# Kernel tuning notes

Measured on AMD Instinct MI355X. Metric: run time of the kernel, lower is better.

The kernel has to match this reference:

```python
import jax, jax.numpy as jnp
import numpy as np

B, S, D = 2, 2048, 1024
H = 16
HD = D // H  # 64
EPS = 1e-6
ROPE_BASE = 10000.0


def _rms_norm(x, w, eps=EPS):
    # torch nn.RMSNorm over last dim
    var = jnp.mean(jnp.square(x), axis=-1, keepdims=True)
    return x * jax.lax.rsqrt(var + eps) * w


def _rope_tables(seq_len, head_dim, base=ROPE_BASE):
    inv_freq = 1.0 / (base ** (jnp.arange(0, head_dim, 2, dtype=jnp.float32) / head_dim))
    t = jnp.arange(seq_len, dtype=jnp.float32)
    freqs = t[:, None] * inv_freq[None, :]            # [S, HD/2]
    emb = jnp.concatenate([freqs, freqs], axis=-1)    # [S, HD]
    return jnp.cos(emb), jnp.sin(emb)


def _rotate_half(x):
    x1, x2 = jnp.split(x, 2, axis=-1)
    return jnp.concatenate([-x2, x1], axis=-1)


def _apply_rope(x, cos, sin):
    # x: [B, H, S, HD]; cos/sin: [S, HD]
    return x * cos[None, None] + _rotate_half(x) * sin[None, None]


def setup_inputs() -> dict:
    key = jax.random.key(0)
    ks = jax.random.split(key, 8)
    scale = 1.0 / np.sqrt(D)
    return {
        "x": jax.random.normal(ks[0], (B, S, D), dtype=jnp.float32),
        "wq": jax.random.normal(ks[1], (D, D), dtype=jnp.float32) * scale,
        "wk": jax.random.normal(ks[2], (D, D), dtype=jnp.float32) * scale,
        "wv": jax.random.normal(ks[3], (D, D), dtype=jnp.float32) * scale,
        "wo": jax.random.normal(ks[4], (D, D), dtype=jnp.float32) * scale,
        "q_norm_w": jnp.ones((HD,), dtype=jnp.float32),
        "k_norm_w": jnp.ones((HD,), dtype=jnp.float32),
        "sink_logit": jnp.zeros((H,), dtype=jnp.float32),
    }


def reference(x, wq, wk, wv, wo, q_norm_w, k_norm_w, sink_logit):
    b, s, _ = x.shape
    # QKV projections (nn.Linear, no bias): y = x @ W^T
    q = jnp.einsum("bsd,od->bso", x, wq).reshape(b, s, H, HD)
    k = jnp.einsum("bsd,od->bso", x, wk).reshape(b, s, H, HD)
    v = jnp.einsum("bsd,od->bso", x, wv).reshape(b, s, H, HD)
    # QK RMSNorm (per head_dim)
    q = _rms_norm(q, q_norm_w)
    k = _rms_norm(k, k_norm_w)
    # [B, H, S, HD]
    q = q.transpose(0, 2, 1, 3)
    k = k.transpose(0, 2, 1, 3)
    v = v.transpose(0, 2, 1, 3)
    # full-head RoPE
    cos, sin = _rope_tables(s, HD)
    q = _apply_rope(q, cos, sin)
    k = _apply_rope(k, cos, sin)
    # manual attention with causal mask and sink softmax
    scale = HD ** -0.5
    scores = jnp.einsum("bhqd,bhkd->bhqk", q, k) * scale  # [B,H,S,S]
    causal = jnp.tril(jnp.ones((s, s), dtype=bool))
    scores = jnp.where(causal[None, None], scores, -jnp.inf)
    # sink-augmented softmax in fp32: append per-head sink logit, softmax, drop sink column
    sink = jnp.broadcast_to(sink_logit.astype(jnp.float32)[None, :, None, None], (b, H, s, 1))
    aug = jnp.concatenate([scores.astype(jnp.float32), sink], axis=-1)
    weights = jax.nn.softmax(aug, axis=-1)[..., :s].astype(scores.dtype)
    out = jnp.einsum("bhqk,bhkd->bhqd", weights, v)
    out = out.transpose(0, 2, 1, 3).reshape(b, s, D)
    return jnp.einsum("bsd,od->bso", out, wo)
```

## Files before the change

### kernel.cpp

```cpp
#include <hip/hip_runtime.h>

#define Bb 2
#define Ss 2048
#define Dd 1024
#define Hh 16
#define HDd 64
#define BS (Bb * Ss)

typedef __attribute__((ext_vector_type(8))) __bf16 bf16x8;
typedef __attribute__((ext_vector_type(8))) unsigned short u16x8;
typedef __attribute__((ext_vector_type(4))) float f32x4;

__device__ __forceinline__ unsigned short f2bf(float f) {
  union { float f; unsigned u; } v; v.f = f;
  unsigned r = v.u + 0x7fffu + ((v.u >> 16) & 1u);
  return (unsigned short)(r >> 16);
}
__device__ __forceinline__ unsigned short f2bf_fast(float f) {
  union { float f; unsigned u; } v; v.f = f;
  return (unsigned short)((v.u + 0x8000u) >> 16);
}

__device__ __forceinline__ void gl_lds16(const void* g, void* l) {
  __builtin_amdgcn_global_load_lds(
      (const __attribute__((address_space(1))) void*)g,
      (__attribute__((address_space(3))) void*)l, 16, 0, 0);
}

__global__ __launch_bounds__(256) void cast_all(
    const float4* __restrict__ x, const float4* __restrict__ wq,
    const float4* __restrict__ wk, const float4* __restrict__ wv,
    const float4* __restrict__ wo, ushort4* __restrict__ xb,
    ushort4* __restrict__ wqkvb, ushort4* __restrict__ wob,
    float* __restrict__ ct, float* __restrict__ st) {
  int i = blockIdx.x * 256 + threadIdx.x;
  const int NX4 = BS * Dd / 4;
  const int NW4 = Dd * Dd / 4;
  const float4* src;
  ushort4* dst;
  int idx;
  if (i < NX4) { src = x; dst = xb; idx = i; }
  else if ((i -= NX4) < NW4) { src = wq; dst = wqkvb; idx = i; }
  else if ((i -= NW4) < NW4) { src = wk; dst = wqkvb + NW4; idx = i; }
  else if ((i -= NW4) < NW4) { src = wv; dst = wqkvb + 2 * NW4; idx = i; }
  else if ((i -= NW4) < NW4) { src = wo; dst = wob; idx = i; }
  else if ((i -= NW4) < Ss * 32) {
    int s = i >> 5, jj = i & 31;
    float freq = __powf(10000.0f, -(float)jj * (1.0f / 32.0f));
    float cs, sn;
    sincosf((float)s * freq, &sn, &cs);
    ct[i] = cs; st[i] = sn;
    return;
  } else return;
  float4 v = src[idx];
  ushort4 o;
  o.x = f2bf(v.x); o.y = f2bf(v.y); o.z = f2bf(v.z); o.w = f2bf(v.w);
  dst[idx] = o;
}

__global__ __launch_bounds__(256, 3) void gemm_qkv(
    const unsigned short* __restrict__ A, const unsigned short* __restrict__ Bw,
    const float* __restrict__ qw, const float* __restrict__ kw,
    const float* __restrict__ ct, const float* __restrict__ st,
    unsigned short* __restrict__ Qb, unsigned short* __restrict__ Kb,
    unsigned short* __restrict__ Vt) {
  __shared__ __align__(16) unsigned short As[128 * 32];
  __shared__ __align__(16) unsigned short Bs[128 * 32];
  const int K = Dd, tid = threadIdx.x;
  const int lane = tid & 63;
  const int quad = lane >> 4;
  const int l16 = lane & 15;
  const int wave = tid >> 6;
  const int wm = (wave >> 1) * 64;
  const int wn = (wave & 1) * 64;
  const int tile_m = blockIdx.y * 128;
  const int tile_n = blockIdx.x * 128;

  const int off0 = tid * 16;
  const int off1 = 4096 + tid * 16;
  const int r0 = tid >> 2, r1 = r0 + 64;
  const int sch = (((tid & 3) ^ ((tid >> 3) & 3)) << 3);
  const int xg = ((quad ^ ((l16 >> 1) & 3)) << 3);

  const unsigned short* Ag0 = A + (size_t)(tile_m + r0) * K + sch;
  const unsigned short* Ag1 = A + (size_t)(tile_m + r1) * K + sch;
  const unsigned short* Bg0 = Bw + (size_t)(tile_n + r0) * K + sch;
  const unsigned short* Bg1 = Bw + (size_t)(tile_n + r1) * K + sch;

  f32x4 zero = {0.f, 0.f, 0.f, 0.f};
  f32x4 acc[4][4];
#pragma unroll
  for (int mi = 0; mi < 4; ++mi)
#pragma unroll
    for (int ni = 0; ni < 4; ++ni) acc[mi][ni] = zero;

  for (int k0 = 0; k0 < K; k0 += 32) {
    gl_lds16(Ag0 + k0, (char*)As + off0);
    gl_lds16(Ag1 + k0, (char*)As + off1);
    gl_lds16(Bg0 + k0, (char*)Bs + off0);
    gl_lds16(Bg1 + k0, (char*)Bs + off1);
    __syncthreads();
    bf16x8 af[4], bfv[4];
#pragma unroll
    for (int mi = 0; mi < 4; ++mi)
      af[mi] = *(const bf16x8*)&As[(wm + mi * 16 + l16) * 32 + xg];
#pragma unroll
    for (int ni = 0; ni < 4; ++ni)
      bfv[ni] = *(const bf16x8*)&Bs[(wn + ni * 16 + l16) * 32 + xg];
#pragma unroll
    for (int mi = 0; mi < 4; ++mi)
#pragma unroll
      for (int ni = 0; ni < 4; ++ni)
        acc[mi][ni] = __builtin_amdgcn_mfma_f32_16x16x32_bf16(
            af[mi], bfv[ni], acc[mi][ni], 0, 0, 0);
    __syncthreads();
  }

  const int type = blockIdx.x >> 3;
  const int h = (((blockIdx.x & 7) << 7) + wn) >> 6;
  const int bb = tile_m >> 11;
  const size_t bh = (size_t)bb * Hh + h;

  if (type == 2) {
#pragma unroll
    for (int mi = 0; mi < 4; ++mi) {
      int s0 = (tile_m + wm + mi * 16 + quad * 4) & (Ss - 1);
#pragma unroll
      for (int ni = 0; ni < 4; ++ni) {
        int d = ni * 16 + l16;
        ushort4 pv;
        pv.x = f2bf(acc[mi][ni][0]);
        pv.y = f2bf(acc[mi][ni][1]);
        pv.z = f2bf(acc[mi][ni][2]);
        pv.w = f2bf(acc[mi][ni][3]);
        *(ushort4*)&Vt[(bh * HDd + d) * Ss + s0] = pv;
      }
    }
  } else {
    const float* wnp = type ? kw : qw;
    unsigned short* Ob = type ? Kb : Qb;
    const float fscale = type ? 1.0f : 0.125f * 1.44269504f;
    float w0[4];
#pragma unroll
    for (int ni = 0; ni < 4; ++ni) w0[ni] = wnp[ni * 16 + l16];
#pragma unroll
    for (int mi = 0; mi < 4; ++mi) {
#pragma unroll
      for (int r = 0; r < 4; ++r) {
        int s = (tile_m + wm + mi * 16 + quad * 4 + r) & (Ss - 1);
        float ss2 = 0.f;
#pragma unroll
        for (int ni = 0; ni < 4; ++ni) ss2 += acc[mi][ni][r] * acc[mi][ni][r];
        ss2 += __shfl_xor(ss2, 1, 64);
        ss2 += __shfl_xor(ss2, 2, 64);
        ss2 += __shfl_xor(ss2, 4, 64);
        ss2 += __shfl_xor(ss2, 8, 64);
        float rr = rsqrtf(ss2 * (1.0f / 64.0f) + 1e-6f) * fscale;
        float c0 = ct[s * 32 + l16], c1 = ct[s * 32 + 16 + l16];
        float sn0 = st[s * 32 + l16], sn1 = st[s * 32 + 16 + l16];
#pragma unroll
        for (int ni = 0; ni < 4; ++ni) {
          float vn = acc[mi][ni][r] * rr * w0[ni];
          float vp = acc[mi][ni ^ 2][r] * rr * w0[ni ^ 2];
          float cs_ = (ni & 1) ? c1 : c0;
          float sn_ = (ni & 1) ? sn1 : sn0;
          float sg = (ni < 2) ? -1.0f : 1.0f;
          Ob[(bh * Ss + s) * HDd + ni * 16 + l16] = f2bf(vn * cs_ + sg * vp * sn_);
        }
      }
    }
  }
}

__global__ __launch_bounds__(256) void gemm_bt2(
    const unsigned short* __restrict__ A, const unsigned short* __restrict__ Bw,
    float* __restrict__ C, int M, int N, int K) {
  __shared__ __align__(16) unsigned short As[128 * 32];
  __shared__ __align__(16) unsigned short Bs[64 * 32];
  const int tid = threadIdx.x;
  const int lane = tid & 63;
  const int quad = lane >> 4;
  const int l16 = lane & 15;
  const int wave = tid >> 6;
  const int wm = (wave >> 1) * 64;
  const int wn = (wave & 1) * 32;
  const int tile_m = blockIdx.y * 128;
  const int tile_n = blockIdx.x * 64;

  const int off0 = tid * 16;
  const int off1 = 4096 + tid * 16;
  const int r0 = tid >> 2, r1 = r0 + 64;
  const int sch = (((tid & 3) ^ ((tid >> 3) & 3)) << 3);
  const int xg = ((quad ^ ((l16 >> 1) & 3)) << 3);

  const unsigned short* Ag0 = A + (size_t)(tile_m + r0) * K + sch;
  const unsigned short* Ag1 = A + (size_t)(tile_m + r1) * K + sch;
  const unsigned short* Bg0 = Bw + (size_t)(tile_n + r0) * K + sch;

  f32x4 zero = {0.f, 0.f, 0.f, 0.f};
  f32x4 acc[4][2];
#pragma unroll
  for (int mi = 0; mi < 4; ++mi)
#pragma unroll
    for (int ni = 0; ni < 2; ++ni) acc[mi][ni] = zero;

  for (int k0 = 0; k0 < K; k0 += 32) {
    gl_lds16(Ag0 + k0, (char*)As + off0);
    gl_lds16(Ag1 + k0, (char*)As + off1);
    gl_lds16(Bg0 + k0, (char*)Bs + off0);
    __syncthreads();
    bf16x8 af[4], bfv[2];
#pragma unroll
    for (int mi = 0; mi < 4; ++mi)
      af[mi] = *(const bf16x8*)&As[(wm + mi * 16 + l16) * 32 + xg];
#pragma unroll
    for (int ni = 0; ni < 2; ++ni)
      bfv[ni] = *(const bf16x8*)&Bs[(wn + ni * 16 + l16) * 32 + xg];
#pragma unroll
    for (int mi = 0; mi < 4; ++mi)
#pragma unroll
      for (int ni = 0; ni < 2; ++ni)
        acc[mi][ni] = __builtin_amdgcn_mfma_f32_16x16x32_bf16(
            af[mi], bfv[ni], acc[mi][ni], 0, 0, 0);
    __syncthreads();
  }

#pragma unroll
  for (int mi = 0; mi < 4; ++mi) {
#pragma unroll
    for (int ni = 0; ni < 2; ++ni) {
      int col = tile_n + wn + ni * 16 + l16;
#pragma unroll
      for (int r = 0; r < 4; ++r) {
        int row = tile_m + wm + mi * 16 + quad * 4 + r;
        C[(size_t)row * N + col] = acc[mi][ni][r];
      }
    }
  }
}

__global__ __launch_bounds__(256, 2) void flash(
    const unsigned short* __restrict__ Qb, const unsigned short* __restrict__ Kb,
    const unsigned short* __restrict__ Vt, const float* __restrict__ sink,
    unsigned short* __restrict__ Ob) {
  __shared__ __align__(16) unsigned short Ks[2][64 * 64];
  __shared__ __align__(16) unsigned short Vs[2][64 * 64];
  __shared__ __align__(16) unsigned short Ps[2][4][16 * 64];

  int tid = threadIdx.x, lane = tid & 63, wave = tid >> 6;
  int quad = lane >> 4, l16 = lane & 15;

  int lid = blockIdx.x;
  int h = (lid & 7) + 8 * ((lid >> 3) & 1);
  int t = (lid >> 4) & 15;
  int b = lid >> 8;
  const int qta = t, qtb = 31 - t;

  const unsigned short* Qg = Qb + ((size_t)(b * Hh + h) * Ss) * HDd;
  const unsigned short* Kg = Kb + ((size_t)(b * Hh + h) * Ss) * HDd;
  const unsigned short* Vg = Vt + ((size_t)(b * Hh + h) * HDd) * Ss;

  int off0 = tid * 16, off1 = 4096 + tid * 16;
  int sr0 = tid >> 3, sr1 = sr0 + 32;
  int sch = ((tid & 7) ^ (sr0 & 7)) * 8;
  int x0 = ((quad ^ (l16 & 7)) * 8);
  int x1 = x0 ^ 32;

  int myqa = qta * 64 + wave * 16 + l16;
  int myqb = qtb * 64 + wave * 16 + l16;

  float sk = sink[h];
  f32x4 zero = {0.f, 0.f, 0.f, 0.f};

  bf16x8 ones;
  {
    u16x8 tt;
#pragma unroll
    for (int i = 0; i < 8; ++i) tt[i] = 0x3F80;
    ones = *(bf16x8*)&tt;
  }

  const unsigned short* Qra = Qg + (size_t)myqa * HDd;
  const unsigned short* Qrb = Qg + (size_t)myqb * HDd;
  bf16x8 aq0a = *(const bf16x8*)(Qra + quad * 8);
  bf16x8 aq1a = *(const bf16x8*)(Qra + 32 + quad * 8);
  bf16x8 aq0b = *(const bf16x8*)(Qrb + quad * 8);
  bf16x8 aq1b = *(const bf16x8*)(Qrb + 32 + quad * 8);

  gl_lds16(Kg + (size_t)sr0 * 64 + sch, (char*)Ks[0] + off0);
  gl_lds16(Kg + (size_t)sr1 * 64 + sch, (char*)Ks[0] + off1);
  gl_lds16(Vg + (size_t)sr0 * Ss + sch, (char*)Vs[0] + off0);
  gl_lds16(Vg + (size_t)sr1 * Ss + sch, (char*)Vs[0] + off1);

  f32x4 Oacca[4], Oaccb[4], lacca = zero, laccb = zero;
#pragma unroll
  for (int ni = 0; ni < 4; ++ni) { Oacca[ni] = zero; Oaccb[ni] = zero; }

  __syncthreads();
  gl_lds16(Kg + (size_t)(64 + sr0) * 64 + sch, (char*)Ks[1] + off0);
  gl_lds16(Kg + (size_t)(64 + sr1) * 64 + sch, (char*)Ks[1] + off1);

  f32x4 sca[4], scb[4];
#pragma unroll
  for (int ni = 0; ni < 4; ++ni) {
    bf16x8 bk0 = *(const bf16x8*)&Ks[0][(ni * 16 + l16) * 64 + x0];
    bf16x8 bk1 = *(const bf16x8*)&Ks[0][(ni * 16 + l16) * 64 + x1];
    scb[ni] = __builtin_amdgcn_mfma_f32_16x16x32_bf16(bk0, aq0b, zero, 0, 0, 0);
    scb[ni] = __builtin_amdgcn_mfma_f32_16x16x32_bf16(bk1, aq1b, scb[ni], 0, 0, 0);
    sca[ni] = __builtin_amdgcn_mfma_f32_16x16x32_bf16(bk0, aq0a, zero, 0, 0, 0);
    sca[ni] = __builtin_amdgcn_mfma_f32_16x16x32_bf16(bk1, aq1a, sca[ni], 0, 0, 0);
  }
  if (qta == 0) {
#pragma unroll
    for (int ni = 0; ni < 4; ++ni)
#pragma unroll
      for (int r = 0; r < 4; ++r)
        if (ni * 16 + quad * 4 + r > myqa) sca[ni][r] = -1.0e38f;
  }

  char* Pwa = (char*)Ps[0][wave];
  char* Pwb = (char*)Ps[1][wave];
  const int prow = l16 * 128;
  const int psw = l16 & 7;

  for (int kt = 0; kt <= qtb; ++kt) {
    bool last = (kt == qtb);
    bool acta = (kt <= qta);
    __syncthreads();
    if (kt + 2 <= qtb) {
      gl_lds16(Kg + (size_t)((kt + 2) * 64 + sr0) * 64 + sch, (char*)Ks[kt & 1] + off0);
      gl_lds16(Kg + (size_t)((kt + 2) * 64 + sr1) * 64 + sch, (char*)Ks[kt & 1] + off1);
    }
    if (kt + 1 <= qtb) {
      gl_lds16(Vg + (size_t)sr0 * Ss + (kt + 1) * 64 + sch, (char*)Vs[(kt + 1) & 1] + off0);
      gl_lds16(Vg + (size_t)sr1 * Ss + (kt + 1) * 64 + sch, (char*)Vs[(kt + 1) & 1] + off1);
    }

#pragma unroll
    for (int ni = 0; ni < 4; ++ni) {
      ushort4 pk;
      pk.x = f2bf_fast(exp2f(scb[ni][0]));
      pk.y = f2bf_fast(exp2f(scb[ni][1]));
      pk.z = f2bf_fast(exp2f(scb[ni][2]));
      pk.w = f2bf_fast(exp2f(scb[ni][3]));
      int chunk = (ni * 2 + (quad >> 1)) ^ psw;
      *(ushort4*)(Pwb + prow + chunk * 16 + (quad & 1) * 8) = pk;
    }
    if (acta) {
#pragma unroll
      for (int ni = 0; ni < 4; ++ni) {
        ushort4 pk;
        pk.x = f2bf_fast(exp2f(sca[ni][0]));
        pk.y = f2bf_fast(exp2f(sca[ni][1]));
        pk.z = f2bf_fast(exp2f(sca[ni][2]));
        pk.w = f2bf_fast(exp2f(sca[ni][3]));
        int chunk = (ni * 2 + (quad >> 1)) ^ psw;
        *(ushort4*)(Pwa + prow + chunk * 16 + (quad & 1) * 8) = pk;
      }
    }

    f32x4 scnb[4], scna[4];
    if (!last) {
      const unsigned short* Kt = Ks[(kt + 1) & 1];
#pragma unroll
      for (int ni = 0; ni < 4; ++ni) {
        bf16x8 bk0 = *(const bf16x8*)&Kt[(ni * 16 + l16) * 64 + x0];
        bf16x8 bk1 = *(const bf16x8*)&Kt[(ni * 16 + l16) * 64 + x1];
        scnb[ni] = __builtin_amdgcn_mfma_f32_16x16x32_bf16(bk0, aq0b, zero, 0, 0, 0);
        scnb[ni] = __builtin_amdgcn_mfma_f32_16x16x32_bf16(bk1, aq1b, scnb[ni], 0, 0, 0);
        if (kt + 1 <= qta) {
          scna[ni] = __builtin_amdgcn_mfma_f32_16x16x32_bf16(bk0, aq0a, zero, 0, 0, 0);
          scna[ni] = __builtin_amdgcn_mfma_f32_16x16x32_bf16(bk1, aq1a, scna[ni], 0, 0, 0);
        }
      }
      if (kt + 1 == qtb) {
#pragma unroll
        for (int ni = 0; ni < 4; ++ni)
#pragma unroll
          for (int r = 0; r < 4; ++r)
            if ((kt + 1) * 64 + ni * 16 + quad * 4 + r > myqb) scnb[ni][r] = -1.0e38f;
      }
      if (kt + 1 == qta) {
#pragma unroll
        for (int ni = 0; ni < 4; ++ni)
#pragma unroll
          for (int r = 0; r < 4; ++r)
            if ((kt + 1) * 64 + ni * 16 + quad * 4 + r > myqa) scna[ni][r] = -1.0e38f;
      }
    }

    asm volatile("s_waitcnt lgkmcnt(0)" ::: "memory");
    bf16x8 ap0b = *(const bf16x8*)(Pwb + prow + ((quad ^ psw) * 16));
    bf16x8 ap1b = *(const bf16x8*)(Pwb + prow + (((quad + 4) ^ psw) * 16));

    const unsigned short* Vtile = Vs[kt & 1];
#pragma unroll
    for (int ni = 0; ni < 4; ++ni) {
      bf16x8 bv0 = *(const bf16x8*)&Vtile[(ni * 16 + l16) * 64 + x0];
      bf16x8 bv1 = *(const bf16x8*)&Vtile[(ni * 16 + l16) * 64 + x1];
      Oaccb[ni] = __builtin_amdgcn_mfma_f32_16x16x32_bf16(bv0, ap0b, Oaccb[ni], 0, 0, 0);
      Oaccb[ni] = __builtin_amdgcn_mfma_f32_16x16x32_bf16(bv1, ap1b, Oaccb[ni], 0, 0, 0);
    }
    laccb = __builtin_amdgcn_mfma_f32_16x16x32_bf16(ones, ap0b, laccb, 0, 0, 0);
    laccb = __builtin_amdgcn_mfma_f32_16x16x32_bf16(ones, ap1b, laccb, 0, 0, 0);

    if (acta) {
      bf16x8 ap0a = *(const bf16x8*)(Pwa + prow + ((quad ^ psw) * 16));
      bf16x8 ap1a = *(const bf16x8*)(Pwa + prow + (((quad + 4) ^ psw) * 16));
#pragma unroll
      for (int ni = 0; ni < 4; ++ni) {
        bf16x8 bv0 = *(const bf16x8*)&Vtile[(ni * 16 + l16) * 64 + x0];
        bf16x8 bv1 = *(const bf16x8*)&Vtile[(ni * 16 + l16) * 64 + x1];
        Oacca[ni] = __builtin_amdgcn_mfma_f32_16x16x32_bf16(bv0, ap0a, Oacca[ni], 0, 0, 0);
        Oacca[ni] = __builtin_amdgcn_mfma_f32_16x16x32_bf16(bv1, ap1a, Oacca[ni], 0, 0, 0);
      }
      lacca = __builtin_amdgcn_mfma_f32_16x16x32_bf16(ones, ap0a, lacca, 0, 0, 0);
      lacca = __builtin_amdgcn_mfma_f32_16x16x32_bf16(ones, ap1a, lacca, 0, 0, 0);
    }

    if (!last) {
#pragma unroll
      for (int ni = 0; ni < 4; ++ni) scb[ni] = scnb[ni];
      if (kt + 1 <= qta) {
#pragma unroll
        for (int ni = 0; ni < 4; ++ni) sca[ni] = scna[ni];
      }
    }
  }

  float sinkw = exp2f(sk * 1.44269504f);
  float inva = 1.0f / (lacca[0] + sinkw);
  float invb = 1.0f / (laccb[0] + sinkw);
#pragma unroll
  for (int ni = 0; ni < 4; ++ni) {
    ushort4 ov;
    ov.x = f2bf(Oacca[ni][0] * inva);
    ov.y = f2bf(Oacca[ni][1] * inva);
    ov.z = f2bf(Oacca[ni][2] * inva);
    ov.w = f2bf(Oacca[ni][3] * inva);
    *(ushort4*)&Ob[((size_t)b * Ss + myqa) * Dd + h * 64 + ni * 16 + quad * 4] = ov;
    ushort4 ow;
    ow.x = f2bf(Oaccb[ni][0] * invb);
    ow.y = f2bf(Oaccb[ni][1] * invb);
    ow.z = f2bf(Oaccb[ni][2] * invb);
    ow.w = f2bf(Oaccb[ni][3] * invb);
    *(ushort4*)&Ob[((size_t)b * Ss + myqb) * Dd + h * 64 + ni * 16 + quad * 4] = ow;
  }
}

extern "C" void kernel_launch(void* const* d_in, const int* in_sizes, int n_in,
                              void* d_out, int out_size, void* d_ws, size_t ws_size,
                              hipStream_t stream) {
  const float* x  = (const float*)d_in[0];
  const float* wq = (const float*)d_in[1];
  const float* wk = (const float*)d_in[2];
  const float* wv = (const float*)d_in[3];
  const float* wo = (const float*)d_in[4];
  const float* qw = (const float*)d_in[5];
  const float* kw = (const float*)d_in[6];
  const float* sk = (const float*)d_in[7];

  char* ws = (char*)d_ws;
  const size_t MB = 1ull << 20;
  unsigned short* xb    = (unsigned short*)(ws + 0);
  unsigned short* attnb = (unsigned short*)(ws + 0);
  unsigned short* wqkvb = (unsigned short*)(ws + 8 * MB);
  unsigned short* wob   = (unsigned short*)(ws + 14 * MB);
  float*          ct    = (float*)(ws + 16 * MB);
  float*          st    = (float*)(ws + 17 * MB);
  unsigned short* Qb    = (unsigned short*)(ws + 40 * MB);
  unsigned short* Kb    = (unsigned short*)(ws + 48 * MB);
  unsigned short* Vt    = (unsigned short*)(ws + 56 * MB);

  cast_all<<<8448, 256, 0, stream>>>(
      (const float4*)x, (const float4*)wq, (const float4*)wk, (const float4*)wv,
      (const float4*)wo, (ushort4*)xb, (ushort4*)wqkvb, (ushort4*)wob, ct, st);
  gemm_qkv<<<dim3(24, 32), 256, 0, stream>>>(xb, wqkvb, qw, kw, ct, st, Qb, Kb, Vt);
  flash<<<dim3(512), 256, 0, stream>>>(Qb, Kb, Vt, sk, attnb);
  gemm_bt2<<<dim3(16, 32), 256, 0, stream>>>(attnb, wob, (float*)d_out, BS, Dd, Dd);
}
```

Before: 190.6 us.

## Double-buffer GEMM tiles, pair adjacent query tiles in flash, raise occupancy

The projection GEMM now double-buffers its LDS tiles, issuing loads for the next K slice before computing the current one. The flash kernel pairs adjacent query tiles (2j, 2j+1) instead of mirrored ones (t, 31-t), so both share almost the entire K/V sweep and their PV MFMAs read each V fragment once. Blocks are scheduled heaviest first, occupancy is hinted at 3 blocks per CU, and s_setprio raises priority around the MFMA region. Pairing adjacent tiles makes per-block work uneven, which relies on the longest-first ordering to balance load. The GEMM loop's trailing __syncthreads is not shown, so the safety of reusing buffers is hard to confirm.

```diff
diff --git a/kernel.cpp b/kernel.cpp
--- a/kernel.cpp
+++ b/kernel.cpp
@@ -175,8 +175,8 @@
 __global__ __launch_bounds__(256) void gemm_bt2(
     const unsigned short* __restrict__ A, const unsigned short* __restrict__ Bw,
     float* __restrict__ C, int M, int N, int K) {
-  __shared__ __align__(16) unsigned short As[128 * 32];
-  __shared__ __align__(16) unsigned short Bs[64 * 32];
+  __shared__ __align__(16) unsigned short As[2][128 * 32];
+  __shared__ __align__(16) unsigned short Bs[2][64 * 32];
   const int tid = threadIdx.x;
   const int lane = tid & 63;
   const int quad = lane >> 4;
@@ -204,18 +204,25 @@
 #pragma unroll
     for (int ni = 0; ni < 2; ++ni) acc[mi][ni] = zero;
 
-  for (int k0 = 0; k0 < K; k0 += 32) {
-    gl_lds16(Ag0 + k0, (char*)As + off0);
-    gl_lds16(Ag1 + k0, (char*)As + off1);
-    gl_lds16(Bg0 + k0, (char*)Bs + off0);
-    __syncthreads();
+  gl_lds16(Ag0, (char*)As[0] + off0);
+  gl_lds16(Ag1, (char*)As[0] + off1);
+  gl_lds16(Bg0, (char*)Bs[0] + off0);
+  __syncthreads();
+
+  int cur = 0;
+  for (int k0 = 0; k0 < K; k0 += 32, cur ^= 1) {
+    if (k0 + 32 < K) {
+      gl_lds16(Ag0 + k0 + 32, (char*)As[cur ^ 1] + off0);
+      gl_lds16(Ag1 + k0 + 32, (char*)As[cur ^ 1] + off1);
+      gl_lds16(Bg0 + k0 + 32, (char*)Bs[cur ^ 1] + off0);
+    }
     bf16x8 af[4], bfv[2];
 #pragma unroll
     for (int mi = 0; mi < 4; ++mi)
-      af[mi] = *(const bf16x8*)&As[(wm + mi * 16 + l16) * 32 + xg];
+      af[mi] = *(const bf16x8*)&As[cur][(wm + mi * 16 + l16) * 32 + xg];
 #pragma unroll
     for (int ni = 0; ni < 2; ++ni)
-      bfv[ni] = *(const bf16x8*)&Bs[(wn + ni * 16 + l16) * 32 + xg];
+      bfv[ni] = *(const bf16x8*)&Bs[cur][(wn + ni * 16 + l16) * 32 + xg];
 #pragma unroll
     for (int mi = 0; mi < 4; ++mi)
 #pragma unroll
@@ -239,7 +246,7 @@
   }
 }
 
-__global__ __launch_bounds__(256, 2) void flash(
+__global__ __launch_bounds__(256, 3) void flash(
     const unsigned short* __restrict__ Qb, const unsigned short* __restrict__ Kb,
     const unsigned short* __restrict__ Vt, const float* __restrict__ sink,
     unsigned short* __restrict__ Ob) {
@@ -251,10 +258,12 @@
   int quad = lane >> 4, l16 = lane & 15;
 
   int lid = blockIdx.x;
-  int h = (lid & 7) + 8 * ((lid >> 3) & 1);
-  int t = (lid >> 4) & 15;
-  int b = lid >> 8;
-  const int qta = t, qtb = 31 - t;
+  int half = lid >> 8, r = lid & 255;
+  int bh = 8 * ((r >> 3) & 3) + (r & 7);
+  int jf = r >> 5;
+  int j = half ? jf : (15 - jf);
+  const int qta = 2 * j, qtb = 2 * j + 1;
+  int b = bh >> 4, h = bh & 15;
 
   const unsigned short* Qg = Qb + ((size_t)(b * Hh + h) * Ss) * HDd;
   const unsigned short* Kg = Kb + ((size_t)(b * Hh + h) * Ss) * HDd;
@@ -267,7 +276,7 @@
   int x1 = x0 ^ 32;
 
   int myqa = qta * 64 + wave * 16 + l16;
-  int myqb = qtb * 64 + wave * 16 + l16;
+  int myqb = myqa + 64;
 
   float sk = sink[h];
   f32x4 zero = {0.f, 0.f, 0.f, 0.f};
@@ -314,8 +323,8 @@
 #pragma unroll
     for (int ni = 0; ni < 4; ++ni)
 #pragma unroll
-      for (int r = 0; r < 4; ++r)
-        if (ni * 16 + quad * 4 + r > myqa) sca[ni][r] = -1.0e38f;
+      for (int r2 = 0; r2 < 4; ++r2)
+        if (ni * 16 + quad * 4 + r2 > myqa) sca[ni][r2] = -1.0e38f;
   }
 
   char* Pwa = (char*)Ps[0][wave];
@@ -325,7 +334,7 @@
 
   for (int kt = 0; kt <= qtb; ++kt) {
     bool last = (kt == qtb);
-    bool acta = (kt <= qta);
+    bool acta = !last;
     __syncthreads();
     if (kt + 2 <= qtb) {
       gl_lds16(Kg + (size_t)((kt + 2) * 64 + sr0) * 64 + sch, (char*)Ks[kt & 1] + off0);
@@ -359,6 +368,7 @@
       }
     }
 
+    __builtin_amdgcn_s_setprio(1);
     f32x4 scnb[4], scna[4];
     if (!last) {
       const unsigned short* Kt = Ks[(kt + 1) & 1];
@@ -377,15 +387,15 @@
 #pragma unroll
         for (int ni = 0; ni < 4; ++ni)
 #pragma unroll
-          for (int r = 0; r < 4; ++r)
-            if ((kt + 1) * 64 + ni * 16 + quad * 4 + r > myqb) scnb[ni][r] = -1.0e38f;
+          for (int r2 = 0; r2 < 4; ++r2)
+            if ((kt + 1) * 64 + ni * 16 + quad * 4 + r2 > myqb) scnb[ni][r2] = -1.0e38f;
       }
       if (kt + 1 == qta) {
 #pragma unroll
         for (int ni = 0; ni < 4; ++ni)
 #pragma unroll
-          for (int r = 0; r < 4; ++r)
-            if ((kt + 1) * 64 + ni * 16 + quad * 4 + r > myqa) scna[ni][r] = -1.0e38f;
+          for (int r2 = 0; r2 < 4; ++r2)
+            if ((kt + 1) * 64 + ni * 16 + quad * 4 + r2 > myqa) scna[ni][r2] = -1.0e38f;
       }
     }
 
@@ -394,16 +404,6 @@
     bf16x8 ap1b = *(const bf16x8*)(Pwb + prow + (((quad + 4) ^ psw) * 16));
 
     const unsigned short* Vtile = Vs[kt & 1];
-#pragma unroll
-    for (int ni = 0; ni < 4; ++ni) {
-      bf16x8 bv0 = *(const bf16x8*)&Vtile[(ni * 16 + l16) * 64 + x0];
-      bf16x8 bv1 = *(const bf16x8*)&Vtile[(ni * 16 + l16) * 64 + x1];
-      Oaccb[ni] = __builtin_amdgcn_mfma_f32_16x16x32_bf16(bv0, ap0b, Oaccb[ni], 0, 0, 0);
-      Oaccb[ni] = __builtin_amdgcn_mfma_f32_16x16x32_bf16(bv1, ap1b, Oaccb[ni], 0, 0, 0);
-    }
-    laccb = __builtin_amdgcn_mfma_f32_16x16x32_bf16(ones, ap0b, laccb, 0, 0, 0);
-    laccb = __builtin_amdgcn_mfma_f32_16x16x32_bf16(ones, ap1b, laccb, 0, 0, 0);
-
     if (acta) {
       bf16x8 ap0a = *(const bf16x8*)(Pwa + prow + ((quad ^ psw) * 16));
       bf16x8 ap1a = *(const bf16x8*)(Pwa + prow + (((quad + 4) ^ psw) * 16));
@@ -411,12 +411,25 @@
       for (int ni = 0; ni < 4; ++ni) {
         bf16x8 bv0 = *(const bf16x8*)&Vtile[(ni * 16 + l16) * 64 + x0];
         bf16x8 bv1 = *(const bf16x8*)&Vtile[(ni * 16 + l16) * 64 + x1];
+        Oaccb[ni] = __builtin_amdgcn_mfma_f32_16x16x32_bf16(bv0, ap0b, Oaccb[ni], 0, 0, 0);
+        Oaccb[ni] = __builtin_amdgcn_mfma_f32_16x16x32_bf16(bv1, ap1b, Oaccb[ni], 0, 0, 0);
         Oacca[ni] = __builtin_amdgcn_mfma_f32_16x16x32_bf16(bv0, ap0a, Oacca[ni], 0, 0, 0);
         Oacca[ni] = __builtin_amdgcn_mfma_f32_16x16x32_bf16(bv1, ap1a, Oacca[ni], 0, 0, 0);
       }
       lacca = __builtin_amdgcn_mfma_f32_16x16x32_bf16(ones, ap0a, lacca, 0, 0, 0);
       lacca = __builtin_amdgcn_mfma_f32_16x16x32_bf16(ones, ap1a, lacca, 0, 0, 0);
-    }
+    } else {
+#pragma unroll
+      for (int ni = 0; ni < 4; ++ni) {
+        bf16x8 bv0 = *(const bf16x8*)&Vtile[(ni * 16 + l16) * 64 + x0];
+        bf16x8 bv1 = *(const bf16x8*)&Vtile[(ni * 16 + l16) * 64 + x1];
+        Oaccb[ni] = __builtin_amdgcn_mfma_f32_16x16x32_bf16(bv0, ap0b, Oaccb[ni], 0, 0, 0);
+        Oaccb[ni] = __builtin_amdgcn_mfma_f32_16x16x32_bf16(bv1, ap1b, Oaccb[ni], 0, 0, 0);
+      }
+    }
+    laccb = __builtin_amdgcn_mfma_f32_16x16x32_bf16(ones, ap0b, laccb, 0, 0, 0);
+    laccb = __builtin_amdgcn_mfma_f32_16x16x32_bf16(ones, ap1b, laccb, 0, 0, 0);
+    __builtin_amdgcn_s_setprio(0);
 
     if (!last) {
 #pragma unroll
```

After: 184.9 us. 1.03x faster.
